# Kernel optimization log

Hardware: AMD Instinct MI355X
Metric: run time of the kernel (lower is better)

The kernel has to match this reference:

```python
import jax, jax.numpy as jnp
import numpy as np

H = 4      # num_attention_heads
DK = 75    # d_k = hidden_size // H
HID = 300  # hidden_size


def setup_inputs() -> dict:
    key = jax.random.key(0)
    ks = jax.random.split(key, 9)
    B, S = 8, 2048
    query = jax.random.normal(ks[0], (B, S, HID), dtype=jnp.float32)
    key_t = jax.random.normal(ks[1], (B, S, HID), dtype=jnp.float32)
    value = jax.random.normal(ks[2], (B, S, HID), dtype=jnp.float32)
    mask = jax.random.randint(ks[3], (B, S), 0, 2, dtype=jnp.int32)
    scale = 1.0 / np.sqrt(HID)
    Wq = jax.random.normal(ks[4], (HID, HID), dtype=jnp.float32) * scale
    Wk = jax.random.normal(ks[5], (HID, HID), dtype=jnp.float32) * scale
    Wv = jax.random.normal(ks[6], (HID, HID), dtype=jnp.float32) * scale
    Wo = jax.random.normal(ks[7], (HID, HID), dtype=jnp.float32) * scale
    bo = jax.random.normal(ks[8], (HID,), dtype=jnp.float32) * 0.01
    return {"query": query, "key": key_t, "value": value, "mask": mask,
            "Wq": Wq, "Wk": Wk, "Wv": Wv, "Wo": Wo, "bo": bo}


def reference(query, key, value, mask, Wq, Wk, Wv, Wo, bo):
    B, S, _ = query.shape
    # QKV projections (nn.Linear: x @ W.T), split into heads: [B,H,S,DK]
    def proj(x, W):
        return (x @ W.T).reshape(B, S, H, DK).transpose(0, 2, 1, 3)
    q, k, v = proj(query, Wq), proj(key, Wk), proj(value, Wv)
    # scores: [B,H,S,S]
    scores = jnp.einsum('bhqd,bhkd->bhqk', q, k) / jnp.sqrt(jnp.float32(DK))
    # mask outer product 'bi,bj->bij' broadcast over heads; fill zeros with -1e9
    m2 = (mask[:, :, None] * mask[:, None, :])[:, None, :, :]  # [B,1,S,S]
    scores = jnp.where(m2 == 0, jnp.float32(-1e9), scores)
    p_attn = jax.nn.softmax(scores, axis=-1)  # dropout p=0.0 (eval mode)
    x = jnp.einsum('bhqk,bhkd->bhqd', p_attn, v)  # [B,H,S,DK]
    x = x.transpose(0, 2, 1, 3).reshape(B, S, H * DK)
    return x @ Wo.T + bo
```

## Files before the change

kernel.cpp:

```cpp
#include <hip/hip_runtime.h>
#include <math.h>

typedef __bf16 bf16x8 __attribute__((ext_vector_type(8)));
typedef float f32x4 __attribute__((ext_vector_type(4)));
typedef float f32x16 __attribute__((ext_vector_type(16)));
typedef unsigned short u16;
typedef u16 u16x8 __attribute__((ext_vector_type(8)));

#define HID 300
#define NH 4
#define DK 75
#define DKP 80
#define BB 8
#define SS 2048
#define BSROWS (BB*SS)
#define C2   0.16658807f

#define MFMA(a,b,c)   __builtin_amdgcn_mfma_f32_16x16x32_bf16(a,b,c,0,0,0)
#define MFMA32(a,b,c) __builtin_amdgcn_mfma_f32_32x32x16_bf16(a,b,c,0,0,0)

static __device__ __forceinline__ void split2(float x, u16& hb, u16& lb) {
    const unsigned u = __float_as_uint(x);
    hb = (u16)(u >> 16);
    const float r = x - __uint_as_float(u & 0xffff0000u);
    lb = (u16)(__float_as_uint(r) >> 16);
}
static __device__ __forceinline__ void split2rne(float x, u16& hb, u16& lb) {
    const unsigned u = __float_as_uint(x);
    const unsigned uh = ((u + 0x7fffu + ((u >> 16) & 1u)) >> 16) << 16;
    hb = (u16)(uh >> 16);
    const float r = x - __uint_as_float(uh);
    lb = (u16)(__float_as_uint(r) >> 16);
}
static __device__ __forceinline__ unsigned pkbf(float a, float b) {
    const unsigned short ua = __builtin_bit_cast(unsigned short, (__bf16)a);
    const unsigned short ub = __builtin_bit_cast(unsigned short, (__bf16)b);
    return (unsigned)ua | ((unsigned)ub << 16);
}

__global__ __launch_bounds__(256)
void prep_w3(const float* __restrict__ Wq, const float* __restrict__ Wk,
             const float* __restrict__ Wv,
             u16* __restrict__ wph, u16* __restrict__ wpl)
{
    const int idx = blockIdx.x * 256 + threadIdx.x;
    if (idx >= 38400) return;
    const int c8 = idx % 40;
    int r = idx / 40;
    const int n = r % 80; r /= 80;
    const int h = r & 3;  r >>= 2;
    const int mat = r;
    const float* W = (mat == 0) ? Wq : (mat == 1) ? Wk : Wv;
    const int col0 = c8 * 8;
    float v[8];
#pragma unroll
    for (int j = 0; j < 8; ++j) v[j] = 0.f;
    if (n < DK) {
        const float* s = W + (size_t)(h * DK + n) * HID + col0;
        if (col0 + 8 <= HID) {
#pragma unroll
            for (int j = 0; j < 8; ++j) v[j] = s[j];
        } else {
#pragma unroll
            for (int j = 0; j < 8; ++j) v[j] = (col0 + j < HID) ? s[j] : 0.f;
        }
    }
    u16x8 hv, lv;
#pragma unroll
    for (int j = 0; j < 8; ++j) {
        u16 hb, lb;
        split2(v[j], hb, lb);
        hv[j] = hb; lv[j] = lb;
    }
    const size_t base = ((size_t)((mat * 4 + h) * 80 + n)) * 320 + col0;
    *(u16x8*)(wph + base) = hv;
    *(u16x8*)(wpl + base) = lv;
}

template <int MODE, int HPB>
static __device__ __forceinline__ void gemm_body(
    char* smem, const float* __restrict__ A, const float* __restrict__ W,
    const u16* __restrict__ Wph, const u16* __restrict__ Wpl,
    const float* __restrict__ bias, u16* __restrict__ hiP, u16* __restrict__ loP,
    float* __restrict__ foutP, const int bx, const int hp,
    const int* __restrict__ pmask, const float scale, const int patch)
{
    constexpr int WROWS = 80 * HPB;
    constexpr int NT = 5 * HPB;
    u16* Ah = (u16*)smem;
    u16* Al = Ah + 128 * 40;
    u16* Wh = Al + 128 * 40;
    u16* Wl = Wh + WROWS * 40;

    const int t = threadIdx.x;
    const int wv = t >> 6, l = t & 63, qc = l & 15, g = l >> 4;
    const int row0 = bx * 128;
    const int b = row0 >> 11;
    const int s0 = row0 & 2047;

    const f32x4 zf = {0.f, 0.f, 0.f, 0.f};
    f32x4 acc[2][NT];
#pragma unroll
    for (int mt = 0; mt < 2; ++mt)
#pragma unroll
        for (int nt = 0; nt < NT; ++nt) acc[mt][nt] = zf;

    const int rA = t >> 1, halfA = t & 1;
    float4 aPf[4];
    constexpr int WJ  = (WROWS * 4 + 255) / 256;
    constexpr int WJ2 = (WROWS * 8 + 255) / 256;
    u16x8 wPfH[WJ], wPfL[WJ];
    float4 wPf2[WJ2];

    auto loadA = [&](int step) {
        const int k0 = step * 32 + halfA * 16;
        const float* src = A + (size_t)(row0 + rA) * HID + k0;
#pragma unroll
        for (int c4 = 0; c4 < 4; ++c4) {
            const int k = k0 + c4 * 4;
            float4 v;
            if (k + 4 <= HID) v = *(const float4*)(src + c4 * 4);
            else {
                v.x = (k + 0 < HID) ? src[c4 * 4 + 0] : 0.f;
                v.y = (k + 1 < HID) ? src[c4 * 4 + 1] : 0.f;
                v.z = (k + 2 < HID) ? src[c4 * 4 + 2] : 0.f;
                v.w = (k + 3 < HID) ? src[c4 * 4 + 3] : 0.f;
            }
            aPf[c4] = v;
        }
    };
    auto loadW = [&](int step) {
        const int k0 = step * 32;
        if constexpr (MODE <= 1) {
#pragma unroll
            for (int j = 0; j < WJ; ++j) {
                const int idx = j * 256 + t;
                if (idx < WROWS * 4) {
                    const int n = idx >> 2, c = idx & 3;
                    const int nh = (n >= 80) ? 1 : 0, nn = n - nh * 80;
                    const size_t wo = (size_t)((hp * HPB + nh) * 80 + nn) * 320 + k0 + c * 8;
                    wPfH[j] = *(const u16x8*)(Wph + wo);
                    wPfL[j] = *(const u16x8*)(Wpl + wo);
                }
            }
        } else {
#pragma unroll
            for (int j = 0; j < WJ2; ++j) {
                const int idx = j * 256 + t;
                if (idx < WROWS * 8) {
                    const int n = idx >> 3, c = idx & 7;
                    const int nh = (n >= 80) ? 1 : 0, nn = n - nh * 80;
                    const int k = k0 + c * 4;
                    float4 v = make_float4(0.f, 0.f, 0.f, 0.f);
                    if (nn < DK) {
                        const float* src = W + (size_t)((hp * HPB + nh) * DK + nn) * HID + k;
                        if (k + 4 <= HID) v = *(const float4*)src;
                        else {
                            v.x = (k + 0 < HID) ? src[0] : 0.f;
                            v.y = (k + 1 < HID) ? src[1] : 0.f;
                            v.z = (k + 2 < HID) ? src[2] : 0.f;
                            v.w = (k + 3 < HID) ? src[3] : 0.f;
                        }
                    }
                    wPf2[j] = v;
                }
            }
        }
    };
    auto writeA = [&]() {
        u16* dh = Ah + rA * 40 + halfA * 16;
        u16* dl = Al + rA * 40 + halfA * 16;
#pragma unroll
        for (int c4 = 0; c4 < 4; ++c4) {
            ushort4 h4, l4;
            split2(aPf[c4].x, h4.x, l4.x);
            split2(aPf[c4].y, h4.y, l4.y);
            split2(aPf[c4].z, h4.z, l4.z);
            split2(aPf[c4].w, h4.w, l4.w);
            *(ushort4*)(dh + c4 * 4) = h4;
            *(ushort4*)(dl + c4 * 4) = l4;
        }
    };
    auto writeW = [&]() {
        if constexpr (MODE <= 1) {
#pragma unroll
            for (int j = 0; j < WJ; ++j) {
                const int idx = j * 256 + t;
                if (idx < WROWS * 4) {
                    const int n = idx >> 2, c = idx & 3;
                    *(u16x8*)(Wh + n * 40 + c * 8) = wPfH[j];
                    *(u16x8*)(Wl + n * 40 + c * 8) = wPfL[j];
                }
            }
        } else {
#pragma unroll
            for (int j = 0; j < WJ2; ++j) {
                const int idx = j * 256 + t;
                if (idx < WROWS * 8) {
                    const int n = idx >> 3, c = idx & 7;
                    ushort4 h4, l4;
                    split2(wPf2[j].x, h4.x, l4.x);
                    split2(wPf2[j].y, h4.y, l4.y);
                    split2(wPf2[j].z, h4.z, l4.z);
                    split2(wPf2[j].w, h4.w, l4.w);
                    *(ushort4*)(Wh + n * 40 + c * 4) = h4;
                    *(ushort4*)(Wl + n * 40 + c * 4) = l4;
                }
            }
        }
    };

    loadA(0);
    loadW(0);

    for (int step = 0; step < 10; ++step) {
        __syncthreads();
        writeA();
        writeW();
        __syncthreads();
        if (step < 9) {
            loadA(step + 1);
            loadW(step + 1);
        }
        bf16x8 ah[2], al2[2];
#pragma unroll
        for (int mt = 0; mt < 2; ++mt) {
            const int roff = (wv * 32 + mt * 16 + qc) * 40 + g * 8;
            ah[mt]  = *(const bf16x8*)(Ah + roff);
            al2[mt] = *(const bf16x8*)(Al + roff);
        }
#pragma unroll
        for (int nt = 0; nt < NT; ++nt) {
            const int woff = (nt * 16 + qc) * 40 + g * 8;
            const bf16x8 bh = *(const bf16x8*)(Wh + woff);
            const bf16x8 bl = *(const bf16x8*)(Wl + woff);
#pragma unroll
            for (int mt = 0; mt < 2; ++mt) {
                acc[mt][nt] = MFMA(ah[mt],  bh, acc[mt][nt]);
                acc[mt][nt] = MFMA(al2[mt], bh, acc[mt][nt]);
                acc[mt][nt] = MFMA(ah[mt],  bl, acc[mt][nt]);
            }
        }
    }
    __syncthreads();

#pragma unroll
    for (int ph = 0; ph < HPB; ++ph) {
        const int h = hp * HPB + ph;
        if constexpr (MODE <= 1) {
            unsigned* epi = (unsigned*)smem;
#pragma unroll
            for (int mt = 0; mt < 2; ++mt)
#pragma unroll
                for (int nt = 0; nt < 5; ++nt)
#pragma unroll
                    for (int r = 0; r < 4; ++r) {
                        u16 hb, lb;
                        split2rne(acc[mt][ph * 5 + nt][r] * scale, hb, lb);
                        if (patch != 0 && nt == 4 && qc == 11) {
                            if (patch == 1) { hb = (u16)0x3F80; lb = 0; }
                            else {
                                const int sr = s0 + wv * 32 + mt * 16 + g * 4 + r;
                                hb = (pmask[b * SS + sr] != 0) ? (u16)0 : (u16)0xC320;
                                lb = 0;
                            }
                        }
                        epi[(wv * 32 + mt * 16 + g * 4 + r) * 84 + nt * 16 + qc] =
                            (unsigned)hb | ((unsigned)lb << 16);
                    }
            __syncthreads();
            if constexpr (MODE == 0) {
                const int r = t >> 1, half = t & 1;
                const unsigned* row = epi + r * 84 + half * 40;
                const size_t base = ((size_t)(b * NH + h) * SS + s0 + r) * DKP + half * 40;
                u16* dh = hiP + base;
#pragma unroll
                for (int i = 0; i < 5; ++i) {
                    u16x8 hv, lv;
#pragma unroll
                    for (int j = 0; j < 8; ++j) {
                        const unsigned u = row[i * 8 + j];
                        hv[j] = (u16)u; lv[j] = (u16)(u >> 16);
                    }
                    *(u16x8*)(dh + i * 8) = hv;
                    if (loP) *(u16x8*)(loP + base + i * 8) = lv;
                }
            } else {
#pragma unroll
                for (int i = 0; i < 3; ++i) {
                    const int idx = i * 256 + t;
                    if (idx < 640) {
                        const int d = idx >> 3, sc = (idx & 7) * 16;
                        const size_t base = ((size_t)(b * NH + h) * DKP + d) * SS + s0 + sc;
                        u16* dh = hiP + base;
                        u16x8 h0, h1, l0, l1;
#pragma unroll
                        for (int j = 0; j < 8; ++j) {
                            unsigned u = epi[(sc + j) * 84 + d];
                            h0[j] = (u16)u; l0[j] = (u16)(u >> 16);
                            u = epi[(sc + 8 + j) * 84 + d];
                            h1[j] = (u16)u; l1[j] = (u16)(u >> 16);
                        }
                        *(u16x8*)dh = h0; *(u16x8*)(dh + 8) = h1;
                        if (loP) {
                            *(u16x8*)(loP + base) = l0;
                            *(u16x8*)(loP + base + 8) = l1;
                        }
                    }
                }
            }
        } else {
            float* epf = (float*)smem;
#pragma unroll
            for (int mt = 0; mt < 2; ++mt)
#pragma unroll
                for (int nt = 0; nt < 5; ++nt)
#pragma unroll
                    for (int r = 0; r < 4; ++r)
                        epf[(wv * 32 + mt * 16 + g * 4 + r) * 84 + nt * 16 + qc] =
                            acc[mt][ph * 5 + nt][r];
            __syncthreads();
            for (int i = 0; i < 38; ++i) {
                const int idx = i * 256 + t;
                if (idx < 128 * DK) {
                    const int r = idx / DK, c = idx - r * DK;
                    foutP[(size_t)(row0 + r) * HID + h * DK + c] = epf[r * 84 + c] + bias[h * DK + c];
                }
            }
        }
        if (ph + 1 < HPB) __syncthreads();
    }
}

__global__ __launch_bounds__(256, 3)
void proj3_gemm(const float* __restrict__ Aq, const float* __restrict__ Ak,
                const float* __restrict__ Av, const int* __restrict__ mask,
                const u16* __restrict__ wph, const u16* __restrict__ wpl,
                u16* __restrict__ qh, u16* __restrict__ ql,
                u16* __restrict__ kh, u16* __restrict__ vh)
{
    __shared__ char smem[46080];
    const int z = blockIdx.z;
    const float* A = (z == 0) ? Aq : (z == 1) ? Ak : Av;
    const size_t WMAT = (size_t)4 * 80 * 320;
    u16* hiP = (z == 0) ? qh : (z == 1) ? kh : vh;
    u16* loP = (z == 0) ? ql : nullptr;
    const float scale = (z == 0) ? C2 : 1.0f;
    const int patch = (z == 0) ? 1 : (z == 1) ? 2 : 0;
    if (z == 2)
        gemm_body<1, 2>(smem, A, nullptr, wph + z * WMAT, wpl + z * WMAT,
                        nullptr, hiP, loP, nullptr, blockIdx.x, blockIdx.y,
                        mask, scale, patch);
    else
        gemm_body<0, 2>(smem, A, nullptr, wph + z * WMAT, wpl + z * WMAT,
                        nullptr, hiP, loP, nullptr, blockIdx.x, blockIdx.y,
                        mask, scale, patch);
}

__global__ __launch_bounds__(256)
void out_gemm(const float* __restrict__ A, const float* __restrict__ W,
              const float* __restrict__ bias, float* __restrict__ out)
{
    __shared__ char smem[43008];
    gemm_body<2, 1>(smem, A, W, nullptr, nullptr, bias, nullptr, nullptr, out,
                    blockIdx.x, blockIdx.y, nullptr, 1.0f, 0);
}

__global__ __launch_bounds__(256, 2)
void attn_mfma32(const u16* __restrict__ qhi, const u16* __restrict__ qlo,
                 const u16* __restrict__ khi, const u16* __restrict__ vhi,
                 const int* __restrict__ mask, float* __restrict__ xout)
{
    __shared__ u16 KsH[2 * 8192];
    __shared__ u16 VsH[2 * 6144];
    __shared__ u16 Ps[4 * 2048];

    const int t = threadIdx.x;
    const int wv = t >> 6;
    const int l = t & 63;
    const int q = l & 31;
    const int hi = l >> 5;

    const int bx = blockIdx.x;
    const int xcd = bx & 7, idx = bx >> 3;
    const int bh = xcd * 4 + (idx & 3);
    const int qt = idx >> 2;
    const int b = bh >> 2;
    const int h = bh & 3;
    const int q0 = qt * 128;

    {
        const int rr = (t >> 4) & 15, o8 = t & 15;
        *(uint2*)(VsH + (80 + rr) * 64 + o8 * 4) = make_uint2(0u, 0u);
        *(uint2*)(VsH + 6144 + (80 + rr) * 64 + o8 * 4) = make_uint2(0u, 0u);
    }

    const size_t planeQK = (size_t)bh * (SS * DKP);
    const int qrow = q0 + wv * 32 + q;
    const int mq = (mask[b * SS + qrow] != 0);
    const u16x8 qm = (u16x8)(u16)(mq ? 0xFFFFu : 0u);

    bf16x8 Qh[5], Ql[5];
    {
        const u16* ph = qhi + planeQK + (size_t)qrow * DKP;
        const u16* pl = qlo + planeQK + (size_t)qrow * DKP;
#pragma unroll
        for (int ch = 0; ch < 5; ++ch) {
            u16x8 ua = *(const u16x8*)(ph + 16 * ch + 8 * hi) & qm;
            u16x8 ub = *(const u16x8*)(pl + 16 * ch + 8 * hi) & qm;
            Qh[ch] = *(bf16x8*)&ua;
            Ql[ch] = *(bf16x8*)&ub;
        }
    }

    const u16* kH = khi + planeQK;
    const u16* vH = vhi + (size_t)bh * (DKP * SS);
    u16* PsW = Ps + wv * 2048;

    int kOff[5], kLds[5], vOff[5], vLds[5];
#pragma unroll
    for (int i = 0; i < 5; ++i) {
        const int gi = t + i * 256;
        const int r = gi / 20, c8 = gi % 20;
        kOff[i] = r * 160 + c8 * 8;
        kLds[i] = r * 256 + ((c8 * 8) ^ ((r & 15) << 4));
        const int d = gi >> 4, cv = gi & 15;
        vOff[i] = d * 4096 + cv * 8;
        vLds[i] = d * 128 + ((cv * 8) ^ ((d & 7) << 4));
    }

    uint2 krA[5], vrA[5], krB[5], vrB[5];
#define LOADT(KT, KR, VR) do { _Pragma("unroll") \
    for (int i = 0; i < 5; ++i) { \
        KR[i] = *(const uint2*)((const char*)kH + (size_t)(KT) * 10240 + kOff[i]); \
        VR[i] = *(const uint2*)((const char*)vH + (size_t)(KT) * 128 + vOff[i]); \
    } } while (0)
#define WRITET(BUF, KR, VR) do { _Pragma("unroll") \
    for (int i = 0; i < 5; ++i) { \
        *(uint2*)((char*)(KsH + (BUF) * 8192) + kLds[i]) = KR[i]; \
        *(uint2*)((char*)(VsH + (BUF) * 6144) + vLds[i]) = VR[i]; \
    } } while (0)

    LOADT(0, krA, vrA);
    WRITET(0, krA, vrA);
    LOADT(1, krA, vrA);
    LOADT(2, krB, vrB);
    __syncthreads();

    f32x16 O[3];
#pragma unroll
    for (int dt = 0; dt < 3; ++dt) O[dt] = (f32x16){};
    float ll = 0.f;
    const int kswz = (q & 15) << 4;
    const int pswz = (q & 7) << 4;

    for (int kt = 0; kt < 32; ++kt) {
        const int cur = kt & 1;
        const char* Kc = (const char*)(KsH + cur * 8192);
        const char* Vc = (const char*)(VsH + cur * 6144);

        f32x16 s0 = (f32x16){}, s1 = (f32x16){};
#pragma unroll
        for (int ch = 0; ch < 5; ++ch) {
            const int o0 = (32 * ch + 16 * hi) ^ kswz;
            const int o1 = (32 * ch + 16 * hi) ^ (((32 + q) & 15) << 4);
            const bf16x8 a0 = *(const bf16x8*)(Kc + q * 256 + o0);
            const bf16x8 a1 = *(const bf16x8*)(Kc + (32 + q) * 256 + o1);
            s0 = MFMA32(a0, Qh[ch], s0);
            s0 = MFMA32(a0, Ql[ch], s0);
            s1 = MFMA32(a1, Qh[ch], s1);
            s1 = MFMA32(a1, Ql[ch], s1);
        }

        float p0 = 0.f, p1 = 0.f, p2 = 0.f, p3 = 0.f;
#pragma unroll
        for (int sb = 0; sb < 2; ++sb) {
            const f32x16 sv = sb ? s1 : s0;
            float e[16];
#pragma unroll
            for (int r = 0; r < 16; r += 4) {
                e[r + 0] = __builtin_amdgcn_exp2f(sv[r + 0]);
                e[r + 1] = __builtin_amdgcn_exp2f(sv[r + 1]);
                e[r + 2] = __builtin_amdgcn_exp2f(sv[r + 2]);
                e[r + 3] = __builtin_amdgcn_exp2f(sv[r + 3]);
                p0 += e[r + 0]; p1 += e[r + 1]; p2 += e[r + 2]; p3 += e[r + 3];
            }
#pragma unroll
            for (int rr = 0; rr < 4; ++rr) {
                uint2 w;
                w.x = pkbf(e[4 * rr + 0], e[4 * rr + 1]);
                w.y = pkbf(e[4 * rr + 2], e[4 * rr + 3]);
                const int o = (sb * 64 + 16 * rr + 8 * hi) ^ pswz;
                *(uint2*)((char*)PsW + q * 128 + o) = w;
            }
        }
        ll += (p0 + p1) + (p2 + p3);

#pragma unroll
        for (int c = 0; c < 4; ++c) {
            const int po = q * 128 + ((32 * c + 16 * hi) ^ pswz);
            const bf16x8 pA = *(const bf16x8*)((char*)PsW + po);
#pragma unroll
            for (int dt = 0; dt < 3; ++dt) {
                const int drow = 32 * dt + q;
                const int vb = drow * 128 + ((32 * c + 16 * hi) ^ ((drow & 7) << 4));
                const bf16x8 vh8 = *(const bf16x8*)(Vc + vb);
                O[dt] = MFMA32(vh8, pA, O[dt]);
            }
        }

        if (kt < 31) {
            if ((kt & 1) == 0) {
                WRITET(cur ^ 1, krA, vrA);
                if (kt < 29) LOADT(kt + 3, krA, vrA);
            } else {
                WRITET(cur ^ 1, krB, vrB);
                if (kt < 29) LOADT(kt + 3, krB, vrB);
            }
        }
        __syncthreads();
    }
#undef LOADT
#undef WRITET

    ll += __shfl_xor(ll, 32);
    {
        const float inv = 1.0f / ll;
        float* o = xout + (size_t)(b * SS + qrow) * HID + h * DK;
#pragma unroll
        for (int dt = 0; dt < 3; ++dt)
#pragma unroll
            for (int r = 0; r < 16; ++r) {
                const int d = 32 * dt + (r & 3) + 8 * (r >> 2) + 4 * hi;
                if (d < DK) o[d] = O[dt][r] * inv;
            }
    }
}

extern "C" void kernel_launch(void* const* d_in, const int* in_sizes, int n_in,
                              void* d_out, int out_size, void* d_ws, size_t ws_size,
                              hipStream_t stream)
{
    const float* query = (const float*)d_in[0];
    const float* key_t = (const float*)d_in[1];
    const float* value = (const float*)d_in[2];
    const int*   mask  = (const int*)d_in[3];
    const float* Wq    = (const float*)d_in[4];
    const float* Wk    = (const float*)d_in[5];
    const float* Wv    = (const float*)d_in[6];
    const float* Wo    = (const float*)d_in[7];
    const float* bo    = (const float*)d_in[8];
    float* out = (float*)d_out;

    const size_t PL = (size_t)BB * NH * SS * DKP;
    u16* qh = (u16*)d_ws;
    u16* ql = qh + PL;
    u16* kh = ql + PL;
    u16* kl = kh + PL;   (void)kl;
    u16* vh = kl + PL;
    u16* vl = vh + PL;
    float* xws = (float*)(vl + PL);
    u16* wph = (u16*)xws;
    u16* wpl = wph + (size_t)3 * 4 * 80 * 320;

    const dim3 blk(256, 1, 1);

    prep_w3<<<150, blk, 0, stream>>>(Wq, Wk, Wv, wph, wpl);

    proj3_gemm<<<dim3(128, 2, 3), blk, 0, stream>>>(query, key_t, value, mask,
                                                    wph, wpl,
                                                    qh, ql, kh, vh);

    attn_mfma32<<<dim3(512, 1, 1), blk, 0, stream>>>(qh, ql, kh, vh, mask, xws);

    out_gemm<<<dim3(128, NH, 1), blk, 0, stream>>>(xws, Wo, bo, out);
}
```

Before: 171.9 us.

## Software-pipeline PV MFMA one tile behind QK with triple-buffered V

Moves the P·V MFMA of each key tile into the next iteration, so it is issued right after that iteration's QK^T MFMAs and ahead of the exp/softmax work. The aim is to overlap matrix-core work with the transcendental and LDS traffic. V gets a third LDS buffer so the delayed tile stays valid, and the zero padding rows are replaced by a small shared zero vector. This holds P fragments in registers across iterations, which raises register pressure, and adds an epilogue for the last tile.

```diff
diff --git a/kernel.cpp b/kernel.cpp
--- a/kernel.cpp
+++ b/kernel.cpp
@@ -372,7 +372,8 @@
                  const int* __restrict__ mask, float* __restrict__ xout)
 {
     __shared__ u16 KsH[2 * 8192];
-    __shared__ u16 VsH[2 * 6144];
+    __shared__ u16 VsH[3 * 5120];
+    __shared__ u16 VsZ[64];
     __shared__ u16 Ps[4 * 2048];
 
     const int t = threadIdx.x;
@@ -389,11 +390,7 @@
     const int h = bh & 3;
     const int q0 = qt * 128;
 
-    {
-        const int rr = (t >> 4) & 15, o8 = t & 15;
-        *(uint2*)(VsH + (80 + rr) * 64 + o8 * 4) = make_uint2(0u, 0u);
-        *(uint2*)(VsH + 6144 + (80 + rr) * 64 + o8 * 4) = make_uint2(0u, 0u);
-    }
+    if (t < 16) *(uint2*)(VsZ + t * 4) = make_uint2(0u, 0u);
 
     const size_t planeQK = (size_t)bh * (SS * DKP);
     const int qrow = q0 + wv * 32 + q;
@@ -435,14 +432,14 @@
         KR[i] = *(const uint2*)((const char*)kH + (size_t)(KT) * 10240 + kOff[i]); \
         VR[i] = *(const uint2*)((const char*)vH + (size_t)(KT) * 128 + vOff[i]); \
     } } while (0)
-#define WRITET(BUF, KR, VR) do { _Pragma("unroll") \
+#define WRITET(KBUF, VBUF, KR, VR) do { _Pragma("unroll") \
     for (int i = 0; i < 5; ++i) { \
-        *(uint2*)((char*)(KsH + (BUF) * 8192) + kLds[i]) = KR[i]; \
-        *(uint2*)((char*)(VsH + (BUF) * 6144) + vLds[i]) = VR[i]; \
+        *(uint2*)((char*)KsH + (KBUF) * 16384 + kLds[i]) = KR[i]; \
+        *(uint2*)((char*)VsH + (VBUF) * 10240 + vLds[i]) = VR[i]; \
     } } while (0)
 
     LOADT(0, krA, vrA);
-    WRITET(0, krA, vrA);
+    WRITET(0, 0, krA, vrA);
     LOADT(1, krA, vrA);
     LOADT(2, krB, vrB);
     __syncthreads();
@@ -453,11 +450,18 @@
     float ll = 0.f;
     const int kswz = (q & 15) << 4;
     const int pswz = (q & 7) << 4;
+    const int drow2 = 64 + q;
+    const int vsw2 = (drow2 & 7) << 4;
+    const int voff2 = drow2 * 128;
+    const bool z2 = (drow2 >= 80);
+
+    bf16x8 pA[4];
+#pragma unroll
+    for (int c = 0; c < 4; ++c) pA[c] = (bf16x8)(__bf16)0.f;
 
     for (int kt = 0; kt < 32; ++kt) {
         const int cur = kt & 1;
-        const char* Kc = (const char*)(KsH + cur * 8192);
-        const char* Vc = (const char*)(VsH + cur * 6144);
+        const char* Kc = (const char*)KsH + cur * 16384;
 
         f32x16 s0 = (f32x16){}, s1 = (f32x16){};
 #pragma unroll
@@ -472,6 +476,25 @@
             s1 = MFMA32(a1, Ql[ch], s1);
         }
 
+        if (kt > 0) {
+            const char* Vp = (const char*)VsH + ((kt + 2) % 3) * 10240;
+#pragma unroll
+            for (int c = 0; c < 4; ++c) {
+#pragma unroll
+                for (int dt = 0; dt < 2; ++dt) {
+                    const int drow = 32 * dt + q;
+                    const int vb = drow * 128 + ((32 * c + 16 * hi) ^ ((drow & 7) << 4));
+                    const bf16x8 vh8 = *(const bf16x8*)(Vp + vb);
+                    O[dt] = MFMA32(vh8, pA[c], O[dt]);
+                }
+                {
+                    const char* b2 = z2 ? (const char*)VsZ : (Vp + voff2);
+                    const bf16x8 vh8 = *(const bf16x8*)(b2 + ((32 * c + 16 * hi) ^ vsw2));
+                    O[2] = MFMA32(vh8, pA[c], O[2]);
+                }
+            }
+        }
+
         float p0 = 0.f, p1 = 0.f, p2 = 0.f, p3 = 0.f;
 #pragma unroll
         for (int sb = 0; sb < 2; ++sb) {
@@ -495,30 +518,42 @@
             }
         }
         ll += (p0 + p1) + (p2 + p3);
-
 #pragma unroll
         for (int c = 0; c < 4; ++c) {
             const int po = q * 128 + ((32 * c + 16 * hi) ^ pswz);
-            const bf16x8 pA = *(const bf16x8*)((char*)PsW + po);
-#pragma unroll
-            for (int dt = 0; dt < 3; ++dt) {
+            pA[c] = *(const bf16x8*)((char*)PsW + po);
+        }
+
+        if (kt < 31) {
+            const int vwb = (kt + 1) % 3;
+            if ((kt & 1) == 0) {
+                WRITET(cur ^ 1, vwb, krA, vrA);
+                if (kt < 29) LOADT(kt + 3, krA, vrA);
+            } else {
+                WRITET(cur ^ 1, vwb, krB, vrB);
+                if (kt < 29) LOADT(kt + 3, krB, vrB);
+            }
+        }
+        __syncthreads();
+    }
+
+    {
+        const char* Vp = (const char*)VsH + (31 % 3) * 10240;
+#pragma unroll
+        for (int c = 0; c < 4; ++c) {
+#pragma unroll
+            for (int dt = 0; dt < 2; ++dt) {
                 const int drow = 32 * dt + q;
                 const int vb = drow * 128 + ((32 * c + 16 * hi) ^ ((drow & 7) << 4));
-                const bf16x8 vh8 = *(const bf16x8*)(Vc + vb);
-                O[dt] = MFMA32(vh8, pA, O[dt]);
-            }
-        }
-
-        if (kt < 31) {
-            if ((kt & 1) == 0) {
-                WRITET(cur ^ 1, krA, vrA);
-                if (kt < 29) LOADT(kt + 3, krA, vrA);
-            } else {
-                WRITET(cur ^ 1, krB, vrB);
-                if (kt < 29) LOADT(kt + 3, krB, vrB);
-            }
-        }
-        __syncthreads();
+                const bf16x8 vh8 = *(const bf16x8*)(Vp + vb);
+                O[dt] = MFMA32(vh8, pA[c], O[dt]);
+            }
+            {
+                const char* b2 = z2 ? (const char*)VsZ : (Vp + voff2);
+                const bf16x8 vh8 = *(const bf16x8*)(b2 + ((32 * c + 16 * hi) ^ vsw2));
+                O[2] = MFMA32(vh8, pA[c], O[2]);
+            }
+        }
     }
 #undef LOADT
 #undef WRITET
```

Measured after the change: 174.7 us. No clear change (+1.6%).
